# Optimization experiments

Measured on AMD Instinct MI355X. Metric: run time of the kernel, lower is better.

Reference implementation:

```python
import jax, jax.numpy as jnp
import numpy as np

N_NODES = 50000
N_EDGES = 800000
D_MODEL = 96
HEADS = 4


def setup_inputs() -> dict:
    key = jax.random.key(0)
    ks = jax.random.split(key, 6)
    scale = 1.0 / np.sqrt(D_MODEL)  # xavier-ish
    return {
        "embeds": jax.random.normal(ks[0], (N_NODES, D_MODEL), dtype=jnp.float32),
        "qW": jax.random.normal(ks[1], (D_MODEL, D_MODEL), dtype=jnp.float32) * scale,
        "kW": jax.random.normal(ks[2], (D_MODEL, D_MODEL), dtype=jnp.float32) * scale,
        "vW": jax.random.normal(ks[3], (D_MODEL, D_MODEL), dtype=jnp.float32) * scale,
        "rows": jax.random.randint(ks[4], (N_EDGES,), 0, N_NODES, dtype=jnp.int32),
        "cols": jax.random.randint(ks[5], (N_EDGES,), 0, N_NODES, dtype=jnp.int32),
    }


def reference(embeds, qW, kW, vW, rows, cols):
    nvar, d = embeds.shape
    dh = d // HEADS
    e = rows.shape[0]
    # edge gathers + per-edge projections  [E, H, dh]
    q = (embeds[rows] @ qW).reshape(e, HEADS, dh)
    k = (embeds[cols] @ kW).reshape(e, HEADS, dh)
    v = (embeds[cols] @ vW).reshape(e, HEADS, dh)
    # per-edge, per-head attention score, clamped
    scores = jnp.clip(jnp.einsum('ehd,ehd->eh', q, k), -10.0, 10.0)
    exp_s = jnp.exp(scores)  # [E, H]
    # scatter-softmax normalizer over destination node (rows)
    norms = jax.ops.segment_sum(exp_s, rows, num_segments=nvar)[rows]  # [E, H]
    w = exp_s / (norms + 1e-8)
    # weighted aggregation back to nodes  [N, H, dh] -> [N, D]
    res = jax.ops.segment_sum(w[:, :, None] * v, rows, num_segments=nvar).reshape(nvar, d)
    return embeds + res
```

## Files before the change

kernel.cpp:

```cpp
#include <hip/hip_runtime.h>

#define DM 96
#define NH 4
#define DH 24
#define CAP 64
#define BSH 8
#define BCAP2 5120
#define ECHUNK 3072

typedef __attribute__((ext_vector_type(8))) __bf16 bf16x8;
typedef __attribute__((ext_vector_type(4))) float f32x4;

__device__ inline unsigned short f2bf(float f) {
    union { float f; unsigned int i; } c; c.f = f;
    unsigned int r = c.i + 0x7FFFu + ((c.i >> 16) & 1u);
    return (unsigned short)(r >> 16);
}
__device__ inline float lo_bf(unsigned int u) { union { unsigned int i; float f; } c; c.i = u << 16; return c.f; }
__device__ inline float hi_bf(unsigned int u) { union { unsigned int i; float f; } c; c.i = u & 0xFFFF0000u; return c.f; }

__global__ __launch_bounds__(256) void scat_kernel(
    const float* __restrict__ qW, const float* __restrict__ kW, const float* __restrict__ vW,
    const int* __restrict__ rows, const int* __restrict__ cols,
    unsigned short* __restrict__ WT,
    int* __restrict__ gbcnt, uint2* __restrict__ bbuf, int e, int nbin)
{
    __shared__ int cnt0[256];
    __shared__ int excl[256];
    __shared__ int gbase[256];
    __shared__ int wsum[4];
    __shared__ uint2 stage[ECHUNK];

    int t = threadIdx.x;

    int gtid = blockIdx.x * 256 + t;
    if (gtid < 3 * DM * DM) {
        int mat = gtid / (DM * DM);
        int rr = gtid - mat * (DM * DM);
        int c = rr / DM, k = rr - c * DM;
        const float* W = (mat == 0) ? qW : (mat == 1) ? kW : vW;
        WT[gtid] = f2bf(W[k * DM + c]);
    }

    cnt0[t] = 0;
    __syncthreads();

    int base = blockIdx.x * ECHUNK;
    int r[12], c[12], lp[12];
    #pragma unroll
    for (int i = 0; i < 12; ++i) {
        int idx = base + i * 256 + t;
        bool ok = idx < e;
        r[i] = ok ? rows[idx] : -1;
        c[i] = ok ? cols[idx] : 0;
        if (ok) lp[i] = atomicAdd(&cnt0[r[i] >> BSH], 1);
    }
    __syncthreads();

    int v = cnt0[t];
    int lane = t & 63, w = t >> 6;
    int x = v;
    #pragma unroll
    for (int o = 1; o < 64; o <<= 1) {
        int y = __shfl_up(x, o);
        if (lane >= o) x += y;
    }
    if (lane == 63) wsum[w] = x;
    __syncthreads();
    int wbase = 0;
    #pragma unroll
    for (int i = 0; i < 4; ++i) if (i < w) wbase += wsum[i];
    int ex = x + wbase - v;
    int total = wsum[0] + wsum[1] + wsum[2] + wsum[3];
    excl[t] = ex;
    if (t < nbin && v > 0) gbase[t] = atomicAdd(&gbcnt[t], v);
    __syncthreads();

    #pragma unroll
    for (int i = 0; i < 12; ++i) {
        if (r[i] >= 0) {
            int b = r[i] >> BSH;
            stage[excl[b] + lp[i]] = make_uint2((unsigned)r[i], (unsigned)c[i]);
        }
    }
    __syncthreads();

    for (int j = t; j < total; j += 256) {
        uint2 rc = stage[j];
        int b = rc.x >> BSH;
        int pos = gbase[b] + (j - excl[b]);
        if (pos < BCAP2) bbuf[(size_t)b * BCAP2 + pos] = rc;
    }
}

__global__ __launch_bounds__(256) void csrproj_kernel(
    const float* __restrict__ emb, const unsigned short* __restrict__ WT,
    unsigned short* __restrict__ Qb, unsigned short* __restrict__ KVb,
    const int* __restrict__ gbcnt, const uint2* __restrict__ bbuf,
    int* __restrict__ cnt, int* __restrict__ pcols, int n, int nproj)
{
    if ((int)blockIdx.x < nproj) {
        int l = threadIdx.x & 63;
        int w = threadIdx.x >> 6;
        int row0 = blockIdx.x * 64 + w * 16;
        int lr = l & 15;
        int lk = l >> 4;
        int arow = row0 + lr; if (arow >= n) arow = n - 1;

        bf16x8 a[3];
        {
            const float4* e4p = (const float4*)(emb + (size_t)arow * DM);
            #pragma unroll
            for (int kb = 0; kb < 3; ++kb) {
                float4 f0 = e4p[kb * 8 + lk * 2];
                float4 f1 = e4p[kb * 8 + lk * 2 + 1];
                union { unsigned short u[8]; bf16x8 b; } cv;
                cv.u[0] = f2bf(f0.x); cv.u[1] = f2bf(f0.y); cv.u[2] = f2bf(f0.z); cv.u[3] = f2bf(f0.w);
                cv.u[4] = f2bf(f1.x); cv.u[5] = f2bf(f1.y); cv.u[6] = f2bf(f1.z); cv.u[7] = f2bf(f1.w);
                a[kb] = cv.b;
            }
        }

        for (int mat = 0; mat < 3; ++mat) {
            const unsigned short* Wm = WT + mat * DM * DM;
            f32x4 acc[6];
            #pragma unroll
            for (int tc = 0; tc < 6; ++tc) acc[tc] = (f32x4){0.f, 0.f, 0.f, 0.f};
            #pragma unroll
            for (int kb = 0; kb < 3; ++kb) {
                #pragma unroll
                for (int tc = 0; tc < 6; ++tc) {
                    union { uint4 u; bf16x8 b; } bv;
                    bv.u = *(const uint4*)&Wm[(size_t)(tc * 16 + lr) * DM + kb * 32 + lk * 8];
                    acc[tc] = __builtin_amdgcn_mfma_f32_16x16x32_bf16(a[kb], bv.b, acc[tc], 0, 0, 0);
                }
            }
            #pragma unroll
            for (int tc = 0; tc < 6; ++tc) {
                #pragma unroll
                for (int r = 0; r < 4; ++r) {
                    int grow = row0 + lk * 4 + r;
                    if (grow < n) {
                        if (mat == 0)
                            Qb[(size_t)grow * DM + tc * 16 + lr] = f2bf(acc[tc][r]);
                        else
                            KVb[(size_t)grow * (2 * DM) + (mat - 1) * DM + tc * 16 + lr] = f2bf(acc[tc][r]);
                    }
                }
            }
        }
    } else {
        __shared__ int lcnt[256];
        int b = blockIdx.x - nproj;
        int t = threadIdx.x;
        lcnt[t] = 0;
        __syncthreads();
        int m = gbcnt[b]; if (m > BCAP2) m = BCAP2;
        const uint2* src = bbuf + (size_t)b * BCAP2;
        int nbase = b << BSH;
        for (int i = t; i < m; i += 256) {
            uint2 rc = src[i];
            int pos = atomicAdd(&lcnt[(int)rc.x - nbase], 1);
            if (pos < CAP) pcols[(size_t)rc.x * CAP + pos] = (int)rc.y;
        }
        __syncthreads();
        int node = nbase + t;
        if (node < n) cnt[node] = lcnt[t];
    }
}

#define RED3(x) { x += __shfl_xor(x, 4); x += __shfl_xor(x, 8); x += __shfl_xor(x, 16); }

__global__ __launch_bounds__(256) void node_kernel(
    const float* __restrict__ emb, const unsigned short* __restrict__ Qb,
    const unsigned short* __restrict__ KVb,
    const int* __restrict__ cnt, const int* __restrict__ pcols,
    float* __restrict__ out, int n)
{
    int wv = (blockIdx.x * 256 + threadIdx.x) >> 6;
    int l = threadIdx.x & 63;
    int s  = (l >> 2) & 7;
    int h  = l & 3;
    int node = wv * 2 + (l >> 5);
    bool valid = node < n;
    int nodec = valid ? node : n - 1;

    int count = cnt[nodec];
    if (count > CAP) count = CAP;
    if (!valid) count = 0;

    int maxc = count;
    maxc = max(maxc, __shfl_xor(maxc, 32));
    int nit = (maxc + 7) >> 3;

    int bb = pcols[(size_t)nodec * CAP + (l & 31)];

    float q[24];
    {
        const uint4* q4 = (const uint4*)(Qb + (size_t)nodec * DM + h * DH);
        #pragma unroll
        for (int t = 0; t < 3; ++t) {
            uint4 u = q4[t];
            unsigned int uw[4] = {u.x, u.y, u.z, u.w};
            #pragma unroll
            for (int j2 = 0; j2 < 4; ++j2) {
                q[t * 8 + j2 * 2]     = lo_bf(uw[j2]);
                q[t * 8 + j2 * 2 + 1] = hi_bf(uw[j2]);
            }
        }
    }

    float a[24];
    #pragma unroll
    for (int i = 0; i < 24; ++i) a[i] = 0.f;
    float denom = 0.f;

    for (int it = 0; it < nit; ++it) {
        int j = it * 8 + s;
        int c = __shfl(bb, (l & 32) + (j & 31));
        if (j >= 32 && j < count) c = pcols[(size_t)node * CAP + j];

        if (j < count) {
            const uint4* kp = (const uint4*)(KVb + (size_t)c * (2 * DM) + h * DH);
            uint4 ku[3] = {kp[0], kp[1], kp[2]};
            uint4 vu[3] = {kp[12], kp[13], kp[14]};

            float dot = 0.f;
            #pragma unroll
            for (int t = 0; t < 3; ++t) {
                unsigned int uw[4] = {ku[t].x, ku[t].y, ku[t].z, ku[t].w};
                #pragma unroll
                for (int j2 = 0; j2 < 4; ++j2)
                    dot += lo_bf(uw[j2]) * q[t * 8 + j2 * 2] + hi_bf(uw[j2]) * q[t * 8 + j2 * 2 + 1];
            }
            dot = fminf(fmaxf(dot, -10.f), 10.f);
            float es = __expf(dot);
            denom += es;
            #pragma unroll
            for (int t = 0; t < 3; ++t) {
                unsigned int uw[4] = {vu[t].x, vu[t].y, vu[t].z, vu[t].w};
                #pragma unroll
                for (int j2 = 0; j2 < 4; ++j2) {
                    a[t * 8 + j2 * 2]     += es * lo_bf(uw[j2]);
                    a[t * 8 + j2 * 2 + 1] += es * hi_bf(uw[j2]);
                }
            }
        }
    }

    RED3(denom)
    #pragma unroll
    for (int i = 0; i < 24; ++i) { RED3(a[i]) }

    if (s == 0 && valid) {
        float sc = 1.f / (denom + 1e-8f);
        const f32x4* e4 = (const f32x4*)(emb + (size_t)node * DM + h * DH);
        f32x4* o4 = (f32x4*)(out + (size_t)node * DM + h * DH);
        #pragma unroll
        for (int t = 0; t < 6; ++t) {
            f32x4 ev = e4[t];
            f32x4 ov;
            ov.x = ev.x + a[t * 4 + 0] * sc;
            ov.y = ev.y + a[t * 4 + 1] * sc;
            ov.z = ev.z + a[t * 4 + 2] * sc;
            ov.w = ev.w + a[t * 4 + 3] * sc;
            o4[t] = ov;
        }
    }
}

extern "C" void kernel_launch(void* const* d_in, const int* in_sizes, int n_in,
                              void* d_out, int out_size, void* d_ws, size_t ws_size,
                              hipStream_t stream) {
    const float* emb = (const float*)d_in[0];
    const float* qW  = (const float*)d_in[1];
    const float* kW  = (const float*)d_in[2];
    const float* vW  = (const float*)d_in[3];
    const int* rows  = (const int*)d_in[4];
    const int* cols  = (const int*)d_in[5];
    float* out = (float*)d_out;

    int n = in_sizes[0] / DM;
    int e = in_sizes[4];
    int nbin = (n + (1 << BSH) - 1) >> BSH;

    unsigned short* KVb = (unsigned short*)d_ws;
    unsigned short* WT  = KVb + (size_t)n * 2 * DM;
    unsigned short* Qb  = WT + 3 * DM * DM;
    int* cnt   = (int*)(Qb + (size_t)n * DM);
    int* gbcnt = cnt + n;
    int* pcols = gbcnt + nbin;
    uint2* bbuf = (uint2*)(pcols + (size_t)n * CAP);

    hipMemsetAsync(gbcnt, 0, (size_t)nbin * sizeof(int), stream);

    int nscat = (e + ECHUNK - 1) / ECHUNK;
    scat_kernel<<<nscat, 256, 0, stream>>>(qW, kW, vW, rows, cols, WT, gbcnt, bbuf, e, nbin);

    int nproj = (n + 63) / 64;
    csrproj_kernel<<<nproj + nbin, 256, 0, stream>>>(emb, WT, Qb, KVb,
                                                     gbcnt, bbuf, cnt, pcols, n, nproj);

    node_kernel<<<(n + 7) / 8, 256, 0, stream>>>(emb, Qb, KVb, cnt, pcols, out, n);
}
```

Before: 92.21 us.

## Merge projection into scatter kernel, stage transposed weights in LDS per block

The node projection moves out of the CSR-build kernel and into the edge-scatter kernel as extra blocks, so projection runs alongside binning instead of after it. The global bf16 transposed-weight buffer is dropped. Each projection block now converts and transposes the three fp32 weight matrices into padded LDS itself, which removes a dependency on the scatter stage. In exchange, every projection block repeats the weight conversion, and LDS use rises to about 27KB per block, which may lower occupancy.

```diff
diff --git a/kernel.cpp b/kernel.cpp
--- a/kernel.cpp
+++ b/kernel.cpp
@@ -7,6 +7,7 @@
 #define BSH 8
 #define BCAP2 5120
 #define ECHUNK 3072
+#define SWP 104
 
 typedef __attribute__((ext_vector_type(8))) __bf16 bf16x8;
 typedef __attribute__((ext_vector_type(4))) float f32x4;
@@ -19,90 +20,80 @@
 __device__ inline float lo_bf(unsigned int u) { union { unsigned int i; float f; } c; c.i = u << 16; return c.f; }
 __device__ inline float hi_bf(unsigned int u) { union { unsigned int i; float f; } c; c.i = u & 0xFFFF0000u; return c.f; }
 
-__global__ __launch_bounds__(256) void scat_kernel(
+__global__ __launch_bounds__(256) void projscat_kernel(
+    const float* __restrict__ emb,
     const float* __restrict__ qW, const float* __restrict__ kW, const float* __restrict__ vW,
     const int* __restrict__ rows, const int* __restrict__ cols,
-    unsigned short* __restrict__ WT,
-    int* __restrict__ gbcnt, uint2* __restrict__ bbuf, int e, int nbin)
+    unsigned short* __restrict__ Qb, unsigned short* __restrict__ KVb,
+    int* __restrict__ gbcnt, uint2* __restrict__ bbuf,
+    int n, int e, int nbin, int nscat)
 {
-    __shared__ int cnt0[256];
-    __shared__ int excl[256];
-    __shared__ int gbase[256];
-    __shared__ int wsum[4];
-    __shared__ uint2 stage[ECHUNK];
-
-    int t = threadIdx.x;
-
-    int gtid = blockIdx.x * 256 + t;
-    if (gtid < 3 * DM * DM) {
-        int mat = gtid / (DM * DM);
-        int rr = gtid - mat * (DM * DM);
-        int c = rr / DM, k = rr - c * DM;
-        const float* W = (mat == 0) ? qW : (mat == 1) ? kW : vW;
-        WT[gtid] = f2bf(W[k * DM + c]);
-    }
-
-    cnt0[t] = 0;
-    __syncthreads();
-
-    int base = blockIdx.x * ECHUNK;
-    int r[12], c[12], lp[12];
-    #pragma unroll
-    for (int i = 0; i < 12; ++i) {
-        int idx = base + i * 256 + t;
-        bool ok = idx < e;
-        r[i] = ok ? rows[idx] : -1;
-        c[i] = ok ? cols[idx] : 0;
-        if (ok) lp[i] = atomicAdd(&cnt0[r[i] >> BSH], 1);
-    }
-    __syncthreads();
-
-    int v = cnt0[t];
-    int lane = t & 63, w = t >> 6;
-    int x = v;
-    #pragma unroll
-    for (int o = 1; o < 64; o <<= 1) {
-        int y = __shfl_up(x, o);
-        if (lane >= o) x += y;
-    }
-    if (lane == 63) wsum[w] = x;
-    __syncthreads();
-    int wbase = 0;
-    #pragma unroll
-    for (int i = 0; i < 4; ++i) if (i < w) wbase += wsum[i];
-    int ex = x + wbase - v;
-    int total = wsum[0] + wsum[1] + wsum[2] + wsum[3];
-    excl[t] = ex;
-    if (t < nbin && v > 0) gbase[t] = atomicAdd(&gbcnt[t], v);
-    __syncthreads();
-
-    #pragma unroll
-    for (int i = 0; i < 12; ++i) {
-        if (r[i] >= 0) {
-            int b = r[i] >> BSH;
-            stage[excl[b] + lp[i]] = make_uint2((unsigned)r[i], (unsigned)c[i]);
-        }
-    }
-    __syncthreads();
-
-    for (int j = t; j < total; j += 256) {
-        uint2 rc = stage[j];
-        int b = rc.x >> BSH;
-        int pos = gbase[b] + (j - excl[b]);
-        if (pos < BCAP2) bbuf[(size_t)b * BCAP2 + pos] = rc;
-    }
-}
-
-__global__ __launch_bounds__(256) void csrproj_kernel(
-    const float* __restrict__ emb, const unsigned short* __restrict__ WT,
-    unsigned short* __restrict__ Qb, unsigned short* __restrict__ KVb,
-    const int* __restrict__ gbcnt, const uint2* __restrict__ bbuf,
-    int* __restrict__ cnt, int* __restrict__ pcols, int n, int nproj)
-{
-    if ((int)blockIdx.x < nproj) {
+    __shared__ __align__(16) unsigned char smem[27712];
+
+    if ((int)blockIdx.x < nscat) {
+        int* cnt0  = (int*)smem;
+        int* excl  = cnt0 + 256;
+        int* gbase = excl + 256;
+        int* wsum  = gbase + 256;
+        uint2* stage = (uint2*)(smem + 3136);
+
+        int t = threadIdx.x;
+        cnt0[t] = 0;
+        __syncthreads();
+
+        int base = blockIdx.x * ECHUNK;
+        int r[12], c[12], lp[12];
+        #pragma unroll
+        for (int i = 0; i < 12; ++i) {
+            int idx = base + i * 256 + t;
+            bool ok = idx < e;
+            r[i] = ok ? rows[idx] : -1;
+            c[i] = ok ? cols[idx] : 0;
+            if (ok) lp[i] = atomicAdd(&cnt0[r[i] >> BSH], 1);
+        }
+        __syncthreads();
+
+        int v = cnt0[t];
+        int lane = t & 63, wv = t >> 6;
+        int x = v;
+        #pragma unroll
+        for (int o = 1; o < 64; o <<= 1) {
+            int y = __shfl_up(x, o);
+            if (lane >= o) x += y;
+        }
+        if (lane == 63) wsum[wv] = x;
+        __syncthreads();
+        int wbase = 0;
+        #pragma unroll
+        for (int i = 0; i < 4; ++i) if (i < wv) wbase += wsum[i];
+        int ex = x + wbase - v;
+        int total = wsum[0] + wsum[1] + wsum[2] + wsum[3];
+        excl[t] = ex;
+        if (t < nbin && v > 0) gbase[t] = atomicAdd(&gbcnt[t], v);
+        __syncthreads();
+
+        #pragma unroll
+        for (int i = 0; i < 12; ++i) {
+            if (r[i] >= 0) {
+                int b = r[i] >> BSH;
+                stage[excl[b] + lp[i]] = make_uint2((unsigned)r[i], (unsigned)c[i]);
+            }
+        }
+        __syncthreads();
+
+        for (int j = t; j < total; j += 256) {
+            uint2 rc = stage[j];
+            int b = rc.x >> BSH;
+            int pos = gbase[b] + (j - excl[b]);
+            if (pos < BCAP2) bbuf[(size_t)b * BCAP2 + pos] = rc;
+        }
+    } else {
+        unsigned short* sW = (unsigned short*)smem;
+
+        int tile = blockIdx.x - nscat;
         int l = threadIdx.x & 63;
         int w = threadIdx.x >> 6;
-        int row0 = blockIdx.x * 64 + w * 16;
+        int row0 = tile * 64 + w * 16;
         int lr = l & 15;
         int lk = l >> 4;
         int arow = row0 + lr; if (arow >= n) arow = n - 1;
@@ -122,7 +113,19 @@
         }
 
         for (int mat = 0; mat < 3; ++mat) {
-            const unsigned short* Wm = WT + mat * DM * DM;
+            const float* W = (mat == 0) ? qW : (mat == 1) ? kW : vW;
+            __syncthreads();
+            for (int i4 = threadIdx.x; i4 < (DM * DM) / 4; i4 += 256) {
+                int i = i4 * 4;
+                int k = i / DM, cc = i - k * DM;
+                float4 v = *(const float4*)(W + i);
+                sW[(cc + 0) * SWP + k] = f2bf(v.x);
+                sW[(cc + 1) * SWP + k] = f2bf(v.y);
+                sW[(cc + 2) * SWP + k] = f2bf(v.z);
+                sW[(cc + 3) * SWP + k] = f2bf(v.w);
+            }
+            __syncthreads();
+
             f32x4 acc[6];
             #pragma unroll
             for (int tc = 0; tc < 6; ++tc) acc[tc] = (f32x4){0.f, 0.f, 0.f, 0.f};
@@ -131,7 +134,7 @@
                 #pragma unroll
                 for (int tc = 0; tc < 6; ++tc) {
                     union { uint4 u; bf16x8 b; } bv;
-                    bv.u = *(const uint4*)&Wm[(size_t)(tc * 16 + lr) * DM + kb * 32 + lk * 8];
+                    bv.u = *(const uint4*)&sW[(size_t)(tc * 16 + lr) * SWP + kb * 32 + lk * 8];
                     acc[tc] = __builtin_amdgcn_mfma_f32_16x16x32_bf16(a[kb], bv.b, acc[tc], 0, 0, 0);
                 }
             }
@@ -149,24 +152,29 @@
                 }
             }
         }
-    } else {
-        __shared__ int lcnt[256];
-        int b = blockIdx.x - nproj;
-        int t = threadIdx.x;
-        lcnt[t] = 0;
-        __syncthreads();
-        int m = gbcnt[b]; if (m > BCAP2) m = BCAP2;
-        const uint2* src = bbuf + (size_t)b * BCAP2;
-        int nbase = b << BSH;
-        for (int i = t; i < m; i += 256) {
-            uint2 rc = src[i];
-            int pos = atomicAdd(&lcnt[(int)rc.x - nbase], 1);
-            if (pos < CAP) pcols[(size_t)rc.x * CAP + pos] = (int)rc.y;
-        }
-        __syncthreads();
-        int node = nbase + t;
-        if (node < n) cnt[node] = lcnt[t];
-    }
+    }
+}
+
+__global__ __launch_bounds__(256) void csr_kernel(
+    const int* __restrict__ gbcnt, const uint2* __restrict__ bbuf,
+    int* __restrict__ cnt, int* __restrict__ pcols, int n)
+{
+    __shared__ int lcnt[256];
+    int b = blockIdx.x;
+    int t = threadIdx.x;
+    lcnt[t] = 0;
+    __syncthreads();
+    int m = gbcnt[b]; if (m > BCAP2) m = BCAP2;
+    const uint2* src = bbuf + (size_t)b * BCAP2;
+    int nbase = b << BSH;
+    for (int i = t; i < m; i += 256) {
+        uint2 rc = src[i];
+        int pos = atomicAdd(&lcnt[(int)rc.x - nbase], 1);
+        if (pos < CAP) pcols[(size_t)rc.x * CAP + pos] = (int)rc.y;
+    }
+    __syncthreads();
+    int node = nbase + t;
+    if (node < n) cnt[node] = lcnt[t];
 }
 
 #define RED3(x) { x += __shfl_xor(x, 4); x += __shfl_xor(x, 8); x += __shfl_xor(x, 16); }
@@ -285,8 +293,7 @@
     int nbin = (n + (1 << BSH) - 1) >> BSH;
 
     unsigned short* KVb = (unsigned short*)d_ws;
-    unsigned short* WT  = KVb + (size_t)n * 2 * DM;
-    unsigned short* Qb  = WT + 3 * DM * DM;
+    unsigned short* Qb  = KVb + (size_t)n * 2 * DM;
     int* cnt   = (int*)(Qb + (size_t)n * DM);
     int* gbcnt = cnt + n;
     int* pcols = gbcnt + nbin;
@@ -295,11 +302,12 @@
     hipMemsetAsync(gbcnt, 0, (size_t)nbin * sizeof(int), stream);
 
     int nscat = (e + ECHUNK - 1) / ECHUNK;
-    scat_kernel<<<nscat, 256, 0, stream>>>(qW, kW, vW, rows, cols, WT, gbcnt, bbuf, e, nbin);
-
     int nproj = (n + 63) / 64;
-    csrproj_kernel<<<nproj + nbin, 256, 0, stream>>>(emb, WT, Qb, KVb,
-                                                     gbcnt, bbuf, cnt, pcols, n, nproj);
+    projscat_kernel<<<nscat + nproj, 256, 0, stream>>>(emb, qW, kW, vW, rows, cols,
+                                                       Qb, KVb, gbcnt, bbuf,
+                                                       n, e, nbin, nscat);
+
+    csr_kernel<<<nbin, 256, 0, stream>>>(gbcnt, bbuf, cnt, pcols, n);
 
     node_kernel<<<(n + 7) / 8, 256, 0, stream>>>(emb, Qb, KVb, cnt, pcols, out, n);
 }
```

Measured after the change: 98.65 us. 1.07x slower.
